# Kernel optimization log

Hardware: AMD Instinct MI355X
Metric: run time of the kernel (lower is better)

The kernel has to match this reference:

```python
import jax, jax.numpy as jnp
import numpy as np

T, H, NH, NKV, HD = 2048, 2048, 16, 4, 128
I, E, TOPK = 4096, 8, 2
EPS = 1e-5
THETA = 10000.0
NEG = -1e9


def rmsnorm(x, w):
    return x * jax.lax.rsqrt(jnp.mean(x * x, axis=-1, keepdims=True) + EPS) * w


def apply_rope(x, pos):
    # neox-style rotary: split head_dim in halves
    half = HD // 2
    inv_freq = 1.0 / (THETA ** (jnp.arange(half, dtype=jnp.float32) / half))
    f = pos.astype(jnp.float32)[:, None] * inv_freq[None, :]      # [T, half]
    cos = jnp.cos(f)[:, None, :]
    sin = jnp.sin(f)[:, None, :]
    x1, x2 = jnp.split(x, 2, axis=-1)
    return jnp.concatenate([x1 * cos - x2 * sin, x2 * cos + x1 * sin], axis=-1)


def setup_inputs() -> dict:
    key = jax.random.key(0)
    ks = jax.random.split(key, 10)
    s = 0.02
    return {
        "positions": jnp.arange(T, dtype=jnp.int32),
        "hidden_states": jax.random.normal(ks[0], (T, H), jnp.float32),
        "residual": jax.random.normal(ks[1], (T, H), jnp.float32),
        "ln1_w": jnp.ones((H,), jnp.float32),
        "ln2_w": jnp.ones((H,), jnp.float32),
        "wq": jax.random.normal(ks[2], (NH * HD, H), jnp.float32) * s,
        "wk": jax.random.normal(ks[3], (NKV * HD, H), jnp.float32) * s,
        "wv": jax.random.normal(ks[4], (NKV * HD, H), jnp.float32) * s,
        "wo": jax.random.normal(ks[5], (H, NH * HD), jnp.float32) * s,
        "gate_w": jax.random.normal(ks[6], (E, H), jnp.float32) * s,
        "w1": jax.random.normal(ks[7], (E, I, H), jnp.float32) * s,
        "w3": jax.random.normal(ks[8], (E, I, H), jnp.float32) * s,
        "w2": jax.random.normal(ks[9], (E, H, I), jnp.float32) * s,
    }


def reference(positions, hidden_states, residual, ln1_w, ln2_w,
              wq, wk, wv, wo, gate_w, w1, w3, w2):
    # fused add + input RMSNorm (vLLM RMSNorm with residual)
    x = hidden_states + residual
    residual = x
    h = rmsnorm(x, ln1_w)

    # attention: QKV proj, RoPE, GQA causal attention, o_proj
    q = (h @ wq.T).reshape(T, NH, HD)
    k = (h @ wk.T).reshape(T, NKV, HD)
    v = (h @ wv.T).reshape(T, NKV, HD)
    q = apply_rope(q, positions)
    k = apply_rope(k, positions)
    rep = NH // NKV
    k = jnp.repeat(k, rep, axis=1)  # [T, NH, HD]
    v = jnp.repeat(v, rep, axis=1)
    scores = jnp.einsum('qhd,khd->hqk', q, k) * (HD ** -0.5)
    causal = jnp.tril(jnp.ones((T, T), bool))
    scores = jnp.where(causal[None, :, :], scores, NEG)
    attn = jax.nn.softmax(scores, axis=-1)
    o = jnp.einsum('hqk,khd->qhd', attn, v).reshape(T, NH * HD)
    o = o @ wo.T

    # fused add + post-attention RMSNorm
    x = o + residual
    residual = x
    h = rmsnorm(x, ln2_w)

    # MoE: router top-k (renormalized) + SwiGLU experts
    logits = h @ gate_w.T                       # [T, E]
    probs = jax.nn.softmax(logits, axis=-1)
    top_w, top_i = jax.lax.top_k(probs, TOPK)
    top_w = top_w / jnp.sum(top_w, axis=-1, keepdims=True)
    coef = jnp.zeros((T, E), h.dtype).at[jnp.arange(T)[:, None], top_i].set(top_w)
    out = jnp.zeros_like(h)
    for e in range(E):
        g = h @ w1[e].T                          # [T, I]
        u = h @ w3[e].T
        out = out + coef[:, e:e + 1] * ((jax.nn.silu(g) * u) @ w2[e].T)
    return (out, residual)
```

## Files before the change

### kernel.cpp

```cpp
#include <hip/hip_runtime.h>
#include <hip/hip_bf16.h>
#include <math.h>


#define T_  2048
#define H_  2048
#define NH  16
#define NKV 4
#define HD  128
#define II_ 4096
#define NE  8
#define EPS 1e-5f
#define PROWS 6144

typedef __bf16 bf16x8 __attribute__((ext_vector_type(8)));
typedef float  f32x4  __attribute__((ext_vector_type(4)));
typedef unsigned short u16;

__device__ __forceinline__ u16 f2b(float f){ __bf16 b = (__bf16)f; return __builtin_bit_cast(u16, b); }
__device__ __forceinline__ float b2f(u16 u){ return (float)__builtin_bit_cast(__bf16, u); }

__device__ __forceinline__ void gll16(const void* g, void* l){
  __builtin_amdgcn_global_load_lds(
      (const __attribute__((address_space(1))) unsigned int*)g,
      (__attribute__((address_space(3))) unsigned int*)l, 16, 0, 0);
}

__device__ __forceinline__ bf16x8 cvt8(f32x4 a, f32x4 b){
  uint4 u;
  u.x = (unsigned)f2b(a[0]) | ((unsigned)f2b(a[1])<<16);
  u.y = (unsigned)f2b(a[2]) | ((unsigned)f2b(a[3])<<16);
  u.z = (unsigned)f2b(b[0]) | ((unsigned)f2b(b[1])<<16);
  u.w = (unsigned)f2b(b[2]) | ((unsigned)f2b(b[3])<<16);
  return __builtin_bit_cast(bf16x8, u);
}

__global__ __launch_bounds__(256) void mx_cvt(const float* __restrict__ s,
                                              u16* __restrict__ d, int n8)
{
  int i = blockIdx.x*256 + threadIdx.x;
  int stride = gridDim.x*256;
  for (; i < n8; i += stride){
    const f32x4* p = (const f32x4*)s + 2*(size_t)i;
    f32x4 a = p[0], b = p[1];
    uint4 u;
    u.x = (unsigned)f2b(a[0]) | ((unsigned)f2b(a[1])<<16);
    u.y = (unsigned)f2b(a[2]) | ((unsigned)f2b(a[3])<<16);
    u.z = (unsigned)f2b(b[0]) | ((unsigned)f2b(b[1])<<16);
    u.w = (unsigned)f2b(b[2]) | ((unsigned)f2b(b[3])<<16);
    ((uint4*)d)[i] = u;
  }
}

__global__ __launch_bounds__(256) void mx_cvt_split(const float* __restrict__ s,
                                                    u16* __restrict__ hi,
                                                    u16* __restrict__ lo, int n8)
{
  int i = blockIdx.x*256 + threadIdx.x;
  int stride = gridDim.x*256;
  for (; i < n8; i += stride){
    const f32x4* p = (const f32x4*)s + 2*(size_t)i;
    f32x4 a = p[0], b = p[1];
    uint4 uh, ul;
    u16 h0,h1,h2,h3;
    h0=f2b(a[0]); h1=f2b(a[1]); h2=f2b(a[2]); h3=f2b(a[3]);
    uh.x = (unsigned)h0 | ((unsigned)h1<<16);
    uh.y = (unsigned)h2 | ((unsigned)h3<<16);
    ul.x = (unsigned)f2b(a[0]-b2f(h0)) | ((unsigned)f2b(a[1]-b2f(h1))<<16);
    ul.y = (unsigned)f2b(a[2]-b2f(h2)) | ((unsigned)f2b(a[3]-b2f(h3))<<16);
    h0=f2b(b[0]); h1=f2b(b[1]); h2=f2b(b[2]); h3=f2b(b[3]);
    uh.z = (unsigned)h0 | ((unsigned)h1<<16);
    uh.w = (unsigned)h2 | ((unsigned)h3<<16);
    ul.z = (unsigned)f2b(b[0]-b2f(h0)) | ((unsigned)f2b(b[1]-b2f(h1))<<16);
    ul.w = (unsigned)f2b(b[2]-b2f(h2)) | ((unsigned)f2b(b[3]-b2f(h3))<<16);
    ((uint4*)hi)[i] = uh;
    ((uint4*)lo)[i] = ul;
  }
}

__global__ void mx_rope_table(const int* __restrict__ pos, float* __restrict__ cosT,
                              float* __restrict__ sinT)
{
  int i = blockIdx.x*256 + threadIdx.x;
  int t = i >> 6, d = i & 63;
  float inv = (float)exp(-((double)d/64.0) * 9.210340371976184);
  float f = (float)pos[t] * inv;
  cosT[i] = cosf(f); sinT[i] = sinf(f);
}

__global__ __launch_bounds__(256) void mx_addnorm(
    const float* __restrict__ a, const float* __restrict__ b,
    const float* __restrict__ gam, float* __restrict__ res_out,
    u16* __restrict__ hi, u16* __restrict__ lo,
    float* __restrict__ hf, u16* __restrict__ hbf, int* __restrict__ mz)
{
  int t = blockIdx.x, tid = threadIdx.x;
  if (mz && t == 0 && tid < 8) mz[tid] = 0;
  const float4* A4 = (const float4*)a + (size_t)t*512;
  const float4* B4 = (const float4*)b + (size_t)t*512;
  float4 va = A4[tid], vb = B4[tid];
  float4 x0; x0.x=va.x+vb.x; x0.y=va.y+vb.y; x0.z=va.z+vb.z; x0.w=va.w+vb.w;
  va = A4[tid+256]; vb = B4[tid+256];
  float4 x1; x1.x=va.x+vb.x; x1.y=va.y+vb.y; x1.z=va.z+vb.z; x1.w=va.w+vb.w;
  float ss = x0.x*x0.x + x0.y*x0.y + x0.z*x0.z + x0.w*x0.w
           + x1.x*x1.x + x1.y*x1.y + x1.z*x1.z + x1.w*x1.w;
  #pragma unroll
  for (int d=32; d; d>>=1) ss += __shfl_down(ss, d);
  __shared__ float red[4];
  if ((tid&63)==0) red[tid>>6] = ss;
  __syncthreads();
  ss = red[0]+red[1]+red[2]+red[3];
  float scale = rsqrtf(ss * (1.f/2048.f) + EPS);
  float4* R4 = (float4*)res_out + (size_t)t*512;
  R4[tid] = x0; R4[tid+256] = x1;
  const float4* G4p = (const float4*)gam;
  float4 g0 = G4p[tid], g1 = G4p[tid+256];
  float4 y0; y0.x=x0.x*scale*g0.x; y0.y=x0.y*scale*g0.y; y0.z=x0.z*scale*g0.z; y0.w=x0.w*scale*g0.w;
  float4 y1; y1.x=x1.x*scale*g1.x; y1.y=x1.y*scale*g1.y; y1.z=x1.z*scale*g1.z; y1.w=x1.w*scale*g1.w;
  if (hf){ float4* H4 = (float4*)hf + (size_t)t*512; H4[tid]=y0; H4[tid+256]=y1; }
  if (hi){
    ushort4 uh, ul;
    uh.x=f2b(y0.x); ul.x=f2b(y0.x-b2f(uh.x));
    uh.y=f2b(y0.y); ul.y=f2b(y0.y-b2f(uh.y));
    uh.z=f2b(y0.z); ul.z=f2b(y0.z-b2f(uh.z));
    uh.w=f2b(y0.w); ul.w=f2b(y0.w-b2f(uh.w));
    ((ushort4*)hi)[(size_t)t*512 + tid] = uh; ((ushort4*)lo)[(size_t)t*512 + tid] = ul;
    uh.x=f2b(y1.x); ul.x=f2b(y1.x-b2f(uh.x));
    uh.y=f2b(y1.y); ul.y=f2b(y1.y-b2f(uh.y));
    uh.z=f2b(y1.z); ul.z=f2b(y1.z-b2f(uh.z));
    uh.w=f2b(y1.w); ul.w=f2b(y1.w-b2f(uh.w));
    ((ushort4*)hi)[(size_t)t*512 + tid+256] = uh; ((ushort4*)lo)[(size_t)t*512 + tid+256] = ul;
  }
  if (hbf){
    ushort4 u0; u0.x=f2b(y0.x); u0.y=f2b(y0.y); u0.z=f2b(y0.z); u0.w=f2b(y0.w);
    ushort4 u1; u1.x=f2b(y1.x); u1.y=f2b(y1.y); u1.z=f2b(y1.z); u1.w=f2b(y1.w);
    ((ushort4*)hbf)[(size_t)t*512 + tid] = u0; ((ushort4*)hbf)[(size_t)t*512 + tid+256] = u1;
  }
}

template<int NX, int NY>
__global__ __launch_bounds__(256,2) void mx_gemm3g(
    const u16* __restrict__ Ah, const u16* __restrict__ Al,
    const u16* __restrict__ Bh, const u16* __restrict__ Bl,
    float* __restrict__ C, int ldc, int K)
{
  __shared__ u16 AhS[128*64], AlS[128*64], BhS[128*64], BlS[128*64];
  int bid = blockIdx.x;
  int xcd = bid & 7, j = bid >> 3;
  int x = j % NX, p = j / NX;
  int y = xcd + 8*p;
  int m0 = x*128, n0 = y*128;
  int tid = threadIdx.x;
  int w = tid>>6, lane = tid&63, wr = w>>1, wc = w&1, g = lane>>4, lr = lane&15;
  f32x4 acc[4][4];
  #pragma unroll
  for (int fm=0;fm<4;fm++)
    #pragma unroll
    for (int fn=0;fn<4;fn++) acc[fm][fn] = (f32x4){0.f,0.f,0.f,0.f};

  for (int k0 = 0; k0 < K; k0 += 64) {
    #pragma unroll
    for (int i=0;i<4;i++){
      int c = i*256 + tid, r = c>>3, ch = c&7;
      int sw = ((ch ^ (r&7))<<3);
      int db = (i*256 + w*64)<<3;
      gll16(Ah + (size_t)(m0+r)*K + k0 + sw, &AhS[db]);
      gll16(Al + (size_t)(m0+r)*K + k0 + sw, &AlS[db]);
      gll16(Bh + (size_t)(n0+r)*K + k0 + sw, &BhS[db]);
      gll16(Bl + (size_t)(n0+r)*K + k0 + sw, &BlS[db]);
    }
    __syncthreads();
    #pragma unroll
    for (int kk=0;kk<2;kk++){
      bf16x8 ah[4], al[4], bh[4], bl[4];
      #pragma unroll
      for (int fm=0;fm<4;fm++){
        int r = wr*64 + fm*16 + lr;
        int ch = ((kk<<2)+g) ^ (r&7);
        ah[fm] = *(const bf16x8*)(&AhS[(r<<6)+(ch<<3)]);
        al[fm] = *(const bf16x8*)(&AlS[(r<<6)+(ch<<3)]);
      }
      #pragma unroll
      for (int fn=0;fn<4;fn++){
        int r = wc*64 + fn*16 + lr;
        int ch = ((kk<<2)+g) ^ (r&7);
        bh[fn] = *(const bf16x8*)(&BhS[(r<<6)+(ch<<3)]);
        bl[fn] = *(const bf16x8*)(&BlS[(r<<6)+(ch<<3)]);
      }
      __builtin_amdgcn_s_setprio(1);
      #pragma unroll
      for (int fm=0;fm<4;fm++)
        #pragma unroll
        for (int fn=0;fn<4;fn++){
          acc[fm][fn] = __builtin_amdgcn_mfma_f32_16x16x32_bf16(ah[fm], bh[fn], acc[fm][fn],0,0,0);
          acc[fm][fn] = __builtin_amdgcn_mfma_f32_16x16x32_bf16(ah[fm], bl[fn], acc[fm][fn],0,0,0);
          acc[fm][fn] = __builtin_amdgcn_mfma_f32_16x16x32_bf16(al[fm], bh[fn], acc[fm][fn],0,0,0);
        }
      __builtin_amdgcn_s_setprio(0);
    }
    __syncthreads();
  }
  #pragma unroll
  for (int fm=0;fm<4;fm++)
    #pragma unroll
    for (int fn=0;fn<4;fn++)
      #pragma unroll
      for (int i=0;i<4;i++){
        size_t rg = (size_t)(m0 + wr*64 + fm*16 + g*4 + i);
        int cg = n0 + wc*64 + fn*16 + lr;
        C[rg*ldc + cg] = acc[fm][fn][i];
      }
}

template<int NX, int NY>
__global__ __launch_bounds__(256) void mx_gemm3(
    const u16* __restrict__ Ah, const u16* __restrict__ Al, int lda,
    const float* __restrict__ B,
    float* __restrict__ C, int ldc, int K)
{
  const int LDT = 72;
  __shared__ u16 Ash[128*LDT], Asl[128*LDT], Bsh[128*LDT], Bsl[128*LDT];
  int bid = blockIdx.x, x, y;
  if constexpr ((NY & 7) == 0) {
    int xcd = bid & 7, j = bid >> 3;
    x = j % NX; int p = j / NX;
    y = xcd + 8*p;
  } else { x = bid % NX; y = bid / NX; }
  int m0 = x*128, n0 = y*128;
  int tid = threadIdx.x;
  int w = tid>>6, lane = tid&63, wr = w>>1, wc = w&1, g = lane>>4, lr = lane&15;
  f32x4 acc[4][4];
  #pragma unroll
  for (int fm=0;fm<4;fm++)
    #pragma unroll
    for (int fn=0;fn<4;fn++) acc[fm][fn] = (f32x4){0.f,0.f,0.f,0.f};
  for (int k0 = 0; k0 < K; k0 += 64) {
    #pragma unroll
    for (int i=0;i<4;i++){
      int c = i*256 + tid, r = c>>3, ch = c&7;
      *(uint4*)(&Ash[r*LDT + ch*8]) = *(const uint4*)(Ah + (size_t)(m0+r)*lda + k0 + ch*8);
      *(uint4*)(&Asl[r*LDT + ch*8]) = *(const uint4*)(Al + (size_t)(m0+r)*lda + k0 + ch*8);
    }
    #pragma unroll
    for (int i=0;i<8;i++){
      int f = i*256 + tid, r = f>>4, c4 = f&15;
      float4 v = *(const float4*)(B + (size_t)(n0+r)*K + k0 + c4*4);
      ushort4 hv, lv;
      hv.x=f2b(v.x); lv.x=f2b(v.x-b2f(hv.x));
      hv.y=f2b(v.y); lv.y=f2b(v.y-b2f(hv.y));
      hv.z=f2b(v.z); lv.z=f2b(v.z-b2f(hv.z));
      hv.w=f2b(v.w); lv.w=f2b(v.w-b2f(hv.w));
      *(ushort4*)(&Bsh[r*LDT + c4*4]) = hv;
      *(ushort4*)(&Bsl[r*LDT + c4*4]) = lv;
    }
    __syncthreads();
    #pragma unroll
    for (int kk=0;kk<2;kk++){
      bf16x8 ah[4], al[4], bh[4], bl[4];
      #pragma unroll
      for (int fm=0;fm<4;fm++){
        int r = wr*64 + fm*16 + lr;
        ah[fm] = *(const bf16x8*)(&Ash[r*LDT + kk*32 + g*8]);
        al[fm] = *(const bf16x8*)(&Asl[r*LDT + kk*32 + g*8]);
      }
      #pragma unroll
      for (int fn=0;fn<4;fn++){
        int r = wc*64 + fn*16 + lr;
        bh[fn] = *(const bf16x8*)(&Bsh[r*LDT + kk*32 + g*8]);
        bl[fn] = *(const bf16x8*)(&Bsl[r*LDT + kk*32 + g*8]);
      }
      __builtin_amdgcn_s_setprio(1);
      #pragma unroll
      for (int fm=0;fm<4;fm++)
        #pragma unroll
        for (int fn=0;fn<4;fn++){
          acc[fm][fn] = __builtin_amdgcn_mfma_f32_16x16x32_bf16(ah[fm], bh[fn], acc[fm][fn],0,0,0);
          acc[fm][fn] = __builtin_amdgcn_mfma_f32_16x16x32_bf16(ah[fm], bl[fn], acc[fm][fn],0,0,0);
          acc[fm][fn] = __builtin_amdgcn_mfma_f32_16x16x32_bf16(al[fm], bh[fn], acc[fm][fn],0,0,0);
        }
      __builtin_amdgcn_s_setprio(0);
    }
    __syncthreads();
  }
  #pragma unroll
  for (int fm=0;fm<4;fm++)
    #pragma unroll
    for (int fn=0;fn<4;fn++)
      #pragma unroll
      for (int i=0;i<4;i++){
        size_t rg = (size_t)(m0 + wr*64 + fm*16 + g*4 + i);
        int cg = n0 + wc*64 + fn*16 + lr;
        C[rg*ldc + cg] = acc[fm][fn][i];
      }
}

template<int NY>
__global__ __launch_bounds__(256,2) void mx_moe_w13(
    const u16* __restrict__ A,
    const u16* __restrict__ B1, const u16* __restrict__ B3,
    u16* __restrict__ Y,
    const int* __restrict__ row_map, const int* __restrict__ meta)
{
  __shared__ u16 As[2][128*32], B1s[2][128*32], B3s[2][128*32];
  int bid = blockIdx.x;
  int xcd = bid & 7, j = bid >> 3;
  int x = j & 15, p = j >> 4;
  int panel = xcd + 8*p;
  int e = panel / NY, y = panel % NY;
  if (x >= meta[16+e]) return;
  int rowbase = meta[8+e] + (x<<7);
  const u16* B1p = B1 + ((size_t)e*II_ + y*128)*H_;
  const u16* B3p = B3 + ((size_t)e*II_ + y*128)*H_;
  int tid = threadIdx.x;
  int w = tid>>6, lane = tid&63, wr = w>>1, wc = w&1, g = lane>>4, lr = lane&15;

  int c0 = tid,       r0 = c0>>2, h0 = ((c0&3) ^ ((r0>>1)&3))<<3;
  int c1 = 256 + tid, r1 = c1>>2, h1 = ((c1&3) ^ ((r1>>1)&3))<<3;
  int grow0 = row_map[rowbase + r0];
  int grow1 = row_map[rowbase + r1];
  const u16* sA0  = A   + (size_t)grow0*H_ + h0;
  const u16* sA1  = A   + (size_t)grow1*H_ + h1;
  const u16* sB10 = B1p + (size_t)r0*H_ + h0;
  const u16* sB11 = B1p + (size_t)r1*H_ + h1;
  const u16* sB30 = B3p + (size_t)r0*H_ + h0;
  const u16* sB31 = B3p + (size_t)r1*H_ + h1;
  int db0 = (w*64)<<3, db1 = (256 + w*64)<<3;

  f32x4 acc1[4][4], acc3[4][4];
  #pragma unroll
  for (int fm=0;fm<4;fm++)
    #pragma unroll
    for (int fn=0;fn<4;fn++){ acc1[fm][fn]=(f32x4){0,0,0,0}; acc3[fm][fn]=(f32x4){0,0,0,0}; }

  auto stage = [&](int buf, int k0){
    gll16(sA0  + k0, &As[buf][db0]);
    gll16(sA1  + k0, &As[buf][db1]);
    gll16(sB10 + k0, &B1s[buf][db0]);
    gll16(sB11 + k0, &B1s[buf][db1]);
    gll16(sB30 + k0, &B3s[buf][db0]);
    gll16(sB31 + k0, &B3s[buf][db1]);
  };
  auto compute = [&](int buf){
    bf16x8 af[4], b1f[4], b3f[4];
    #pragma unroll
    for (int fm=0;fm<4;fm++){
      int r = wr*64 + fm*16 + lr;
      int ch = g ^ ((r>>1)&3);
      af[fm] = *(const bf16x8*)(&As[buf][r*32 + (ch<<3)]);
    }
    #pragma unroll
    for (int fn=0;fn<4;fn++){
      int r = wc*64 + fn*16 + lr;
      int ch = g ^ ((r>>1)&3);
      b1f[fn] = *(const bf16x8*)(&B1s[buf][r*32 + (ch<<3)]);
      b3f[fn] = *(const bf16x8*)(&B3s[buf][r*32 + (ch<<3)]);
    }
    __builtin_amdgcn_s_setprio(1);
    #pragma unroll
    for (int fm=0;fm<4;fm++)
      #pragma unroll
      for (int fn=0;fn<4;fn++){
        acc1[fm][fn] = __builtin_amdgcn_mfma_f32_16x16x32_bf16(af[fm], b1f[fn], acc1[fm][fn],0,0,0);
        acc3[fm][fn] = __builtin_amdgcn_mfma_f32_16x16x32_bf16(af[fm], b3f[fn], acc3[fm][fn],0,0,0);
      }
    __builtin_amdgcn_s_setprio(0);
  };

  const int nt = H_ >> 5;
  stage(0, 0);
  for (int t=0; t<nt; ++t){
    int cur = t & 1;
    if (t+1 < nt){
      stage(cur^1, (t+1)<<5);
      asm volatile("s_waitcnt vmcnt(6)" ::: "memory");
    } else {
      asm volatile("s_waitcnt vmcnt(0)" ::: "memory");
    }
    __builtin_amdgcn_s_barrier();
    compute(cur);
    asm volatile("s_waitcnt lgkmcnt(0)" ::: "memory");
    __builtin_amdgcn_s_barrier();
  }

  int n0 = y*128 + wc*64;
  #pragma unroll
  for (int fm=0;fm<4;fm++)
    #pragma unroll
    for (int fn=0;fn<4;fn++)
      #pragma unroll
      for (int i=0;i<4;i++){
        size_t rg = (size_t)(rowbase + wr*64 + fm*16 + g*4 + i);
        int cg = n0 + fn*16 + lr;
        float gg = acc1[fm][fn][i], uu = acc3[fm][fn][i];
        float sg = gg / (1.f + __expf(-gg));
        Y[rg*II_ + cg] = f2b(sg * uu);
      }
}

template<int NY>
__global__ __launch_bounds__(256,2) void mx_moe_w2k(
    const u16* __restrict__ A,
    const u16* __restrict__ B,
    float* __restrict__ C,
    const int* __restrict__ meta)
{
  __shared__ u16 As[128*64], Bs[128*64];
  int bid = blockIdx.x;
  int xcd = bid & 7, j = bid >> 3;
  int x = j & 15, p = j >> 4;
  int panel = xcd + 8*p;
  int e = panel / NY, y = panel % NY;
  if (x >= meta[16+e]) return;
  int rowbase = meta[8+e] + (x<<7);
  const u16* Bp = B + ((size_t)e*H_ + y*128)*II_;
  int tid = threadIdx.x;
  int w = tid>>6, lane = tid&63, wr = w>>1, wc = w&1, g = lane>>4, lr = lane&15;

  f32x4 acc[4][4];
  #pragma unroll
  for (int fm=0;fm<4;fm++)
    #pragma unroll
    for (int fn=0;fn<4;fn++) acc[fm][fn] = (f32x4){0,0,0,0};

  for (int k0 = 0; k0 < II_; k0 += 64) {
    #pragma unroll
    for (int i=0;i<4;i++){
      int c = i*256 + tid, r = c>>3, ch = c&7;
      int sw = (ch ^ (r&7))<<3;
      int db = (i*256 + w*64)<<3;
      gll16(A  + (size_t)(rowbase + r)*II_ + k0 + sw, &As[db]);
      gll16(Bp + (size_t)r*II_             + k0 + sw, &Bs[db]);
    }
    __syncthreads();
    #pragma unroll
    for (int kk=0;kk<2;kk++){
      bf16x8 af[4], bf[4];
      #pragma unroll
      for (int fm=0;fm<4;fm++){
        int r = wr*64 + fm*16 + lr;
        int ch = ((kk<<2)+g) ^ (r&7);
        af[fm] = *(const bf16x8*)(&As[(r<<6)+(ch<<3)]);
      }
      #pragma unroll
      for (int fn=0;fn<4;fn++){
        int r = wc*64 + fn*16 + lr;
        int ch = ((kk<<2)+g) ^ (r&7);
        bf[fn] = *(const bf16x8*)(&Bs[(r<<6)+(ch<<3)]);
      }
      __builtin_amdgcn_s_setprio(1);
      #pragma unroll
      for (int fm=0;fm<4;fm++)
        #pragma unroll
        for (int fn=0;fn<4;fn++)
          acc[fm][fn] = __builtin_amdgcn_mfma_f32_16x16x32_bf16(af[fm], bf[fn], acc[fm][fn],0,0,0);
      __builtin_amdgcn_s_setprio(0);
    }
    __syncthreads();
  }
  int n0 = y*128 + wc*64;
  #pragma unroll
  for (int fm=0;fm<4;fm++)
    #pragma unroll
    for (int fn=0;fn<4;fn++)
      #pragma unroll
      for (int i=0;i<4;i++){
        size_t rg = (size_t)(rowbase + wr*64 + fm*16 + g*4 + i);
        int cg = n0 + fn*16 + lr;
        C[rg*H_ + cg] = acc[fm][fn][i];
      }
}

template<int GATHER, int CBF16, int NYT, int SPLITY>
__global__ __launch_bounds__(512,4) void mx_moe10(
    const u16* __restrict__ A, int lda,
    const float* __restrict__ B1, const float* __restrict__ B2, long long strideB,
    void* __restrict__ C1v, void* __restrict__ C2v, int ldc, int K,
    const int* __restrict__ row_map, const int* __restrict__ meta)
{
  __shared__ u16 AS[3][256*32];
  int bid = blockIdx.x;
  int xcd = bid & 7, j = bid >> 3;
  int x = j & 7, q = j >> 3;
  int panel = xcd + 8*q;
  int e = panel / NYT, y = panel % NYT;
  if (x >= meta[16+e]) return;
  int rowbase = meta[8+e] + x*256;
  int yy = (y < SPLITY) ? y : y - SPLITY;
  const float* Bp = ((y < SPLITY) ? B1 : B2) + (long long)e*strideB + (size_t)(yy*128)*K;
  void* Cv = (y < SPLITY) ? C1v : C2v;
  int tid = threadIdx.x;
  int w = tid>>6, lane = tid&63, wr = w>>2, wc = w&3, g = lane>>4, lr = lane&15;
  const u16 *srcA0, *srcA1;
  {
    int c0 = tid,     r0 = c0>>2;
    int c1 = 512+tid, r1 = c1>>2;
    int s0 = (c0&3) ^ ((r0>>1)&3);
    int s1 = (c1&3) ^ ((r1>>1)&3);
    int w0 = GATHER ? row_map[rowbase+r0] : (rowbase+r0);
    int w1r = GATHER ? row_map[rowbase+r1] : (rowbase+r1);
    srcA0 = A + (size_t)w0*lda + s0*8;
    srcA1 = A + (size_t)w1r*lda + s1*8;
  }
  const float *srcB0, *srcB1;
  {
    int r0 = wc*32 + lr;
    int r1 = wc*32 + 16 + lr;
    srcB0 = Bp + (size_t)r0*K + g*8;
    srcB1 = Bp + (size_t)r1*K + g*8;
  }
  f32x4 acc[8][2];
  #pragma unroll
  for (int fm=0;fm<8;fm++){ acc[fm][0]=(f32x4){0,0,0,0}; acc[fm][1]=(f32x4){0,0,0,0}; }
  f32x4 e0,e1,e2,e3, o0,o1,o2,o3;
  u16 *pa0=&AS[0][0], *pa1=&AS[1][0], *pa2=&AS[2][0];
  int nt = K >> 5;
  auto stageA = [&](u16* as, int k0){
    gll16(srcA0 + k0, as + (w*64)*8);
    gll16(srcA1 + k0, as + (512 + w*64)*8);
  };
  auto issueB = [&](int k0, f32x4& b0, f32x4& b1, f32x4& b2, f32x4& b3){
    b0 = *(const f32x4*)(srcB0 + k0);
    b1 = *(const f32x4*)(srcB0 + k0 + 4);
    b2 = *(const f32x4*)(srcB1 + k0);
    b3 = *(const f32x4*)(srcB1 + k0 + 4);
  };
  auto compute = [&](const u16* as, f32x4 b0, f32x4 b1, f32x4 b2, f32x4 b3){
    bf16x8 bf0 = cvt8(b0,b1), bf1 = cvt8(b2,b3);
    __builtin_amdgcn_s_setprio(1);
    #pragma unroll
    for (int fm=0;fm<8;fm++){
      int r = wr*128 + fm*16 + lr;
      int ch = g ^ ((r>>1)&3);
      bf16x8 af = *(const bf16x8*)(as + r*32 + ch*8);
      acc[fm][0] = __builtin_amdgcn_mfma_f32_16x16x32_bf16(af, bf0, acc[fm][0],0,0,0);
      acc[fm][1] = __builtin_amdgcn_mfma_f32_16x16x32_bf16(af, bf1, acc[fm][1],0,0,0);
    }
    __builtin_amdgcn_s_setprio(0);
  };
  auto rot = [&](){ u16* t0=pa0; pa0=pa1; pa1=pa2; pa2=t0; };
  auto kclamp = [&](int t){ return (t < nt ? t : 0) << 5; };
  issueB(0, e0,e1,e2,e3);
  asm volatile("" ::: "memory");
  stageA(pa0, 0);
  asm volatile("" ::: "memory");
  stageA(pa1, kclamp(1));
  for (int t=0; t<nt; t+=2){
    asm volatile("s_waitcnt vmcnt(2)" ::: "memory");
    __builtin_amdgcn_s_barrier();
    issueB(kclamp(t+1), o0,o1,o2,o3);
    asm volatile("" ::: "memory");
    stageA(pa2, kclamp(t+2));
    compute(pa0, e0,e1,e2,e3);
    rot();
    asm volatile("s_waitcnt vmcnt(2)" ::: "memory");
    __builtin_amdgcn_s_barrier();
    issueB(kclamp(t+2), e0,e1,e2,e3);
    asm volatile("" ::: "memory");
    stageA(pa2, kclamp(t+3));
    compute(pa0, o0,o1,o2,o3);
    rot();
  }
  int n0 = yy*128 + wc*32;
  #pragma unroll
  for (int fm=0;fm<8;fm++)
    #pragma unroll
    for (int fn=0;fn<2;fn++)
      #pragma unroll
      for (int i=0;i<4;i++){
        size_t rg = (size_t)(rowbase + wr*128 + fm*16 + g*4 + i);
        int cg = n0 + fn*16 + lr;
        if (CBF16) ((u16*)Cv)[rg*ldc + cg] = f2b(acc[fm][fn][i]);
        else       ((float*)Cv)[rg*ldc + cg] = acc[fm][fn][i];
      }
}

__global__ __launch_bounds__(256) void mx_rope_apply(const float* __restrict__ qkv,
    const float* __restrict__ cosT, const float* __restrict__ sinT,
    u16* __restrict__ qh, u16* __restrict__ ql, u16* __restrict__ kh, u16* __restrict__ kl)
{
  int t = blockIdx.x*4 + (threadIdx.x>>6);
  int hh = blockIdx.y, d = threadIdx.x & 63;
  const float* row = qkv + (size_t)t*3072;
  float c = cosT[t*64+d], s = sinT[t*64+d];
  float x1, x2; size_t base; u16 *oh, *ol;
  if (hh < NH){ x1 = row[hh*HD+d]; x2 = row[hh*HD+d+64];
     base = ((size_t)hh*T_ + t)*HD; oh = qh; ol = ql; }
  else { int kvh = hh-NH; x1 = row[2048 + kvh*HD + d]; x2 = row[2048 + kvh*HD + d + 64];
     base = ((size_t)kvh*T_ + t)*HD; oh = kh; ol = kl; }
  float o1 = x1*c - x2*s, o2 = x2*c + x1*s;
  u16 a = f2b(o1); oh[base+d]    = a; ol[base+d]    = f2b(o1 - b2f(a));
  u16 b = f2b(o2); oh[base+d+64] = b; ol[base+d+64] = f2b(o2 - b2f(b));
}

__global__ void mx_transpose_v(const float* __restrict__ qkv,
                               u16* __restrict__ vh, u16* __restrict__ vl)
{
  __shared__ float tile[64][132];
  int kv = blockIdx.x, t0 = blockIdx.y*64, tid = threadIdx.x;
  #pragma unroll
  for (int it=0; it<32; ++it){
    int idx = it*256 + tid; int r = idx>>7, d = idx&127;
    tile[r][d] = qkv[(size_t)(t0+r)*3072 + 2560 + kv*HD + d];
  }
  __syncthreads();
  #pragma unroll
  for (int it=0; it<32; ++it){
    int idx = it*256 + tid; int d = idx>>6, j = idx&63;
    float x = tile[j][d];
    u16 a = f2b(x);
    size_t o = ((size_t)kv*HD + d)*T_ + t0 + j;
    vh[o] = a; vl[o] = f2b(x - b2f(a));
  }
}

__global__ __launch_bounds__(256) void mx_attn(
  const u16* __restrict__ qh_, const u16* __restrict__ ql_,
  const u16* __restrict__ kh_, const u16* __restrict__ kl_,
  const u16* __restrict__ vh_, const u16* __restrict__ vl_,
  u16* __restrict__ oh_, u16* __restrict__ ol_)
{
  int h = blockIdx.y, kvh = h >> 2;
  int qt = (h & 8) ? (31 - (int)blockIdx.x) : (int)blockIdx.x;
  int tid = threadIdx.x, w = tid>>6, lane = tid&63, g = lane>>4, lr = lane&15;
  int q0 = qt*64 + w*16;
  __shared__ u16 KV[2][4][8192];
  __shared__ u16 Ph[4][1024], Pl[4][1024];

  bf16x8 qfh[4], qfl[4];
  const u16* qrh = qh_ + ((size_t)h*T_ + q0 + lr)*HD;
  const u16* qrl = ql_ + ((size_t)h*T_ + q0 + lr)*HD;
  #pragma unroll
  for (int kk=0;kk<4;kk++){
    qfh[kk] = *(const bf16x8*)(qrh + kk*32 + g*8);
    qfl[kk] = *(const bf16x8*)(qrl + kk*32 + g*8);
  }
  f32x4 o[8];
  #pragma unroll
  for (int nf=0;nf<8;nf++) o[nf] = (f32x4){0.f,0.f,0.f,0.f};
  float mreg[4] = {-3e38f,-3e38f,-3e38f,-3e38f}, lsum[4] = {0.f,0.f,0.f,0.f};

  const u16* kbase = kh_ + (size_t)kvh*T_*HD;
  const u16* lbase = kl_ + (size_t)kvh*T_*HD;
  const u16* vbase = vh_ + (size_t)kvh*HD*T_;
  const u16* wbase = vl_ + (size_t)kvh*HD*T_;

  auto stage = [&](int buf, int kvb){
    #pragma unroll
    for (int i=0;i<4;i++){
      int cb = i*256 + w*64;
      int c  = cb + lane;
      int kr = c>>4, kc = ((c&15) ^ (kr&7))<<3;
      gll16(kbase + (size_t)(kvb+kr)*HD + kc, &KV[buf][0][cb*8]);
      gll16(lbase + (size_t)(kvb+kr)*HD + kc, &KV[buf][1][cb*8]);
      int vr = c>>3, vc = ((c&7) ^ (vr&7))<<3;
      gll16(vbase + (size_t)vr*T_ + kvb + vc, &KV[buf][2][cb*8]);
      gll16(wbase + (size_t)vr*T_ + kvb + vc, &KV[buf][3][cb*8]);
    }
  };

  stage(0, 0);

  for (int kt = 0; kt <= qt; ++kt) {
    int cur = kt & 1;
    int kvb = kt*64;
    if (kt < qt) {
      stage(cur^1, kvb+64);
      asm volatile("s_waitcnt vmcnt(16)" ::: "memory");
    } else {
      asm volatile("s_waitcnt vmcnt(0)" ::: "memory");
    }
    __builtin_amdgcn_s_barrier();

    f32x4 s[4];
    #pragma unroll
    for (int nf=0;nf<4;nf++) s[nf] = (f32x4){0.f,0.f,0.f,0.f};
    __builtin_amdgcn_s_setprio(1);
    #pragma unroll
    for (int nf=0; nf<4; nf++){
      int row = nf*16 + lr;
      #pragma unroll
      for (int kk=0;kk<4;kk++){
        int off = row*128 + ((((kk<<2)+g) ^ (lr&7))<<3);
        bf16x8 kf = *(const bf16x8*)(&KV[cur][0][off]);
        bf16x8 kg = *(const bf16x8*)(&KV[cur][1][off]);
        s[nf] = __builtin_amdgcn_mfma_f32_16x16x32_bf16(qfh[kk], kf, s[nf],0,0,0);
        s[nf] = __builtin_amdgcn_mfma_f32_16x16x32_bf16(qfh[kk], kg, s[nf],0,0,0);
        s[nf] = __builtin_amdgcn_mfma_f32_16x16x32_bf16(qfl[kk], kf, s[nf],0,0,0);
      }
    }
    __builtin_amdgcn_s_setprio(0);

    float sv[4][4], pm[4];
    #pragma unroll
    for (int i=0;i<4;i++) pm[i] = -3e38f;
    bool diag = (kt == qt);
    #pragma unroll
    for (int nf=0;nf<4;nf++)
      #pragma unroll
      for (int i=0;i<4;i++){
        float v = s[nf][i] * 0.08838834764831845f;
        if (diag && (kvb + nf*16 + lr > q0 + g*4 + i)) v = -1e30f;
        sv[nf][i] = v;
        pm[i] = fmaxf(pm[i], v);
      }
    #pragma unroll
    for (int i=0;i<4;i++)
      #pragma unroll
      for (int d=1; d<16; d<<=1) pm[i] = fmaxf(pm[i], __shfl_xor(pm[i], d));
    float sf[4], psum[4];
    #pragma unroll
    for (int i=0;i<4;i++){
      float nm = fmaxf(mreg[i], pm[i]);
      sf[i] = __expf(mreg[i] - nm);
      mreg[i] = nm; psum[i] = 0.f;
    }
    #pragma unroll
    for (int nf=0;nf<4;nf++)
      #pragma unroll
      for (int i=0;i<4;i++){
        float e = __expf(sv[nf][i] - mreg[i]);
        sv[nf][i] = e; psum[i] += e;
      }
    #pragma unroll
    for (int i=0;i<4;i++){
      #pragma unroll
      for (int d=1; d<16; d<<=1) psum[i] += __shfl_xor(psum[i], d);
      lsum[i] = lsum[i]*sf[i] + psum[i];
    }
    #pragma unroll
    for (int nf=0;nf<8;nf++)
      #pragma unroll
      for (int i=0;i<4;i++) o[nf][i] *= sf[i];

    #pragma unroll
    for (int nf=0;nf<4;nf++)
      #pragma unroll
      for (int i=0;i<4;i++){
        int qi = g*4 + i, kv = nf*16 + lr;
        int idx = qi*64 + (kv ^ ((qi&7)<<3));
        u16 hb = f2b(sv[nf][i]);
        Ph[w][idx] = hb;
        Pl[w][idx] = f2b(sv[nf][i] - b2f(hb));
      }

    #pragma unroll
    for (int kk2=0; kk2<2; kk2++){
      int pidx = lr*64 + ((kk2*32 + g*8) ^ ((lr&7)<<3));
      bf16x8 ph = *(const bf16x8*)(&Ph[w][pidx]);
      bf16x8 pl = *(const bf16x8*)(&Pl[w][pidx]);
      __builtin_amdgcn_s_setprio(1);
      #pragma unroll
      for (int nf=0; nf<8; nf++){
        int row = nf*16 + lr;
        int off = row*64 + ((((kk2<<2)+g) ^ (lr&7))<<3);
        bf16x8 vf = *(const bf16x8*)(&KV[cur][2][off]);
        bf16x8 vg = *(const bf16x8*)(&KV[cur][3][off]);
        o[nf] = __builtin_amdgcn_mfma_f32_16x16x32_bf16(ph, vf, o[nf],0,0,0);
        o[nf] = __builtin_amdgcn_mfma_f32_16x16x32_bf16(ph, vg, o[nf],0,0,0);
        o[nf] = __builtin_amdgcn_mfma_f32_16x16x32_bf16(pl, vf, o[nf],0,0,0);
      }
      __builtin_amdgcn_s_setprio(0);
    }
    __builtin_amdgcn_s_barrier();
  }

  float inv[4];
  #pragma unroll
  for (int i=0;i<4;i++) inv[i] = 1.0f / lsum[i];
  #pragma unroll
  for (int nf=0;nf<8;nf++)
    #pragma unroll
    for (int i=0;i<4;i++){
      float v = o[nf][i] * inv[i];
      size_t oidx = (size_t)(q0 + g*4 + i)*2048 + h*HD + nf*16 + lr;
      u16 hb = f2b(v);
      oh_[oidx] = hb; ol_[oidx] = f2b(v - b2f(hb));
    }
}

__global__ __launch_bounds__(256) void mx_router(
    const float* __restrict__ h2, const float* __restrict__ gw,
    int* __restrict__ meta, int* __restrict__ tki, float* __restrict__ tkw)
{
  int t = blockIdx.x, tid = threadIdx.x;
  float p[8] = {0,0,0,0,0,0,0,0};
  const float* row = h2 + (size_t)t*H_;
  for (int i = tid; i < H_; i += 256) {
    float x = row[i];
    #pragma unroll
    for (int e=0;e<8;e++) p[e] += x * gw[e*H_ + i];
  }
  #pragma unroll
  for (int e=0;e<8;e++)
    #pragma unroll
    for (int d=32; d; d>>=1) p[e] += __shfl_down(p[e], d);
  __shared__ float red[4][8];
  int w = tid>>6;
  if ((tid&63)==0){
    #pragma unroll
    for (int e=0;e<8;e++) red[w][e] = p[e];
  }
  __syncthreads();
  if (tid==0){
    float lg[8];
    #pragma unroll
    for (int e=0;e<8;e++) lg[e] = red[0][e]+red[1][e]+red[2][e]+red[3][e];
    int e0 = 0;
    for (int e=1;e<8;e++) if (lg[e] > lg[e0]) e0 = e;
    int e1 = (e0==0)?1:0;
    for (int e=0;e<8;e++) if (e!=e0 && lg[e] > lg[e1]) e1 = e;
    float w0 = 1.f/(1.f + __expf(lg[e1]-lg[e0]));
    tki[t*2]=e0; tki[t*2+1]=e1; tkw[t*2]=w0; tkw[t*2+1]=1.f-w0;
    atomicAdd(&meta[e0],1); atomicAdd(&meta[e1],1);
  }
}

__global__ void mx_scan(int* __restrict__ meta, int* __restrict__ perm, int gsh)
{
  if (threadIdx.x == 0){
    int run = 0;
    for (int e=0;e<8;e++){
      meta[8+e] = run;
      int pt = (meta[e] + (1<<gsh) - 1) >> gsh;
      meta[16+e] = pt;
      run += pt << gsh;
      meta[24+e] = 0;
    }
  }
  for (int i = threadIdx.x; i < PROWS; i += 256) perm[i] = 0;
}

__global__ void mx_scatter(const int* __restrict__ tki, int* __restrict__ meta,
                           int* __restrict__ perm, int* __restrict__ slot)
{
  int t = blockIdx.x*256 + threadIdx.x;
  if (t >= T_) return;
  #pragma unroll
  for (int j=0;j<2;j++){
    int e = tki[t*2+j];
    int s = atomicAdd(&meta[24+e], 1);
    int pos = meta[8+e] + s;
    perm[pos] = t;
    slot[t*2+j] = pos;
  }
}

__global__ void mx_silu(u16* __restrict__ y1, const u16* __restrict__ y3)
{
  size_t base = ((size_t)blockIdx.x*256 + threadIdx.x)*8;
  uint4 a = *(uint4*)(y1+base);
  uint4 b = *(const uint4*)(y3+base);
  u16* ap = (u16*)&a; u16* bp = (u16*)&b;
  uint4 r; u16* rp = (u16*)&r;
  #pragma unroll
  for (int j=0;j<8;j++){
    float gg = b2f(ap[j]), uu = b2f(bp[j]);
    float sg = gg / (1.f + __expf(-gg));
    rp[j] = f2b(sg * uu);
  }
  *(uint4*)(y1+base) = r;
}

__global__ void mx_combine(const float* __restrict__ Y2, const int* __restrict__ slot,
                           const float* __restrict__ tkw, float* __restrict__ out)
{
  int t = blockIdx.x, tid = threadIdx.x;
  int s0 = slot[t*2], s1 = slot[t*2+1];
  float w0 = tkw[t*2], w1 = tkw[t*2+1];
  const float4* r0 = (const float4*)(Y2 + (size_t)s0*H_);
  const float4* r1 = (const float4*)(Y2 + (size_t)s1*H_);
  float4* o4 = (float4*)(out + (size_t)t*H_);
  for (int i = tid; i < 512; i += 256){
    float4 a = r0[i], b = r1[i], c;
    c.x = w0*a.x + w1*b.x; c.y = w0*a.y + w1*b.y;
    c.z = w0*a.z + w1*b.z; c.w = w0*a.w + w1*b.w;
    o4[i] = c;
  }
}

extern "C" void kernel_launch(void* const* d_in, const int* in_sizes, int n_in,
                              void* d_out, int out_size, void* d_ws, size_t ws_size,
                              hipStream_t stream)
{
  (void)in_sizes; (void)n_in; (void)out_size;
  const int*   positions = (const int*)  d_in[0];
  const float* hidden    = (const float*)d_in[1];
  const float* residual  = (const float*)d_in[2];
  const float* ln1       = (const float*)d_in[3];
  const float* ln2       = (const float*)d_in[4];
  const float* wq        = (const float*)d_in[5];
  const float* wk        = (const float*)d_in[6];
  const float* wv        = (const float*)d_in[7];
  const float* wo        = (const float*)d_in[8];
  const float* gatew     = (const float*)d_in[9];
  const float* w1        = (const float*)d_in[10];
  const float* w3        = (const float*)d_in[11];
  const float* w2        = (const float*)d_in[12];
  float* outp = (float*)d_out;
  char* ws = (char*)d_ws;

  size_t off = 0;
  auto alloc = [&](size_t n){ size_t o = off; off += (n + 255) & ~(size_t)255; return o; };
  float* cosT = (float*)(ws + alloc((size_t)T_*64*4));
  float* sinT = (float*)(ws + alloc((size_t)T_*64*4));
  size_t res1_off = alloc((size_t)T_*H_*4);
  float* res1 = (float*)(ws + res1_off);
  u16*   h1h  = (u16*)  (ws + alloc((size_t)T_*H_*2));
  u16*   h1l  = (u16*)  (ws + alloc((size_t)T_*H_*2));
  float* qkvF = (float*)(ws + alloc((size_t)T_*3072*4));
  size_t qh_off = alloc((size_t)NH*T_*HD*2);
  u16*   qh   = (u16*)  (ws + qh_off);
  u16*   ql   = (u16*)  (ws + alloc((size_t)NH*T_*HD*2));
  u16*   kh   = (u16*)  (ws + alloc((size_t)NKV*T_*HD*2));
  u16*   kl   = (u16*)  (ws + alloc((size_t)NKV*T_*HD*2));
  u16*   vh   = (u16*)  (ws + alloc((size_t)NKV*T_*HD*2));
  u16*   vl   = (u16*)  (ws + alloc((size_t)NKV*T_*HD*2));
  u16*   aoh  = (u16*)  (ws + alloc((size_t)T_*2048*2));
  u16*   aol  = (u16*)  (ws + alloc((size_t)T_*2048*2));
  float* oF   = (float*)(ws + alloc((size_t)T_*H_*4));
  float* h2f  = (float*)(ws + alloc((size_t)T_*H_*4));
  u16*   h2b  = (u16*)  (ws + alloc((size_t)T_*H_*2));
  int*   meta = (int*)  (ws + alloc(32*4));
  int*   tki  = (int*)  (ws + alloc((size_t)T_*2*4));
  float* tkw  = (float*)(ws + alloc((size_t)T_*2*4));
  int*   slot = (int*)  (ws + alloc((size_t)T_*2*4));
  int*   perm = (int*)  (ws + alloc((size_t)PROWS*4));
  u16*   Y1   = (u16*)  (ws + alloc((size_t)PROWS*II_*2));
  u16*   Y3   = (u16*)  (ws + res1_off);
  float* Y2   = (float*)(ws + qh_off);
  u16* w1b = (u16*)(ws + alloc((size_t)NE*II_*H_*2));
  u16* w3b = (u16*)(ws + alloc((size_t)NE*II_*H_*2));
  u16* w2b = (u16*)(ws + alloc((size_t)NE*H_*II_*2));
  u16* qwh = (u16*)(ws + alloc((size_t)3072*H_*2));
  u16* qwl = (u16*)(ws + alloc((size_t)3072*H_*2));
  u16* woh = (u16*)(ws + alloc((size_t)H_*H_*2));
  u16* wol = (u16*)(ws + alloc((size_t)H_*H_*2));
  bool big = ws_size >= off;

  if (big){
    int n8 = NE*II_*H_/8;
    mx_cvt<<<2048, 256, 0, stream>>>(w1, w1b, n8);
    mx_cvt<<<2048, 256, 0, stream>>>(w3, w3b, n8);
    mx_cvt<<<2048, 256, 0, stream>>>(w2, w2b, n8);
    mx_cvt_split<<<512, 256, 0, stream>>>(wq, qwh,                qwl,                2048*2048/8);
    mx_cvt_split<<<512, 256, 0, stream>>>(wk, qwh + 2048*2048,    qwl + 2048*2048,    512*2048/8);
    mx_cvt_split<<<512, 256, 0, stream>>>(wv, qwh + 2560*2048,    qwl + 2560*2048,    512*2048/8);
    mx_cvt_split<<<512, 256, 0, stream>>>(wo, woh,                wol,                2048*2048/8);
  }
  mx_rope_table<<<512, 256, 0, stream>>>(positions, cosT, sinT);
  mx_addnorm<<<T_, 256, 0, stream>>>(hidden, residual, ln1, res1, h1h, h1l,
                                     nullptr, nullptr, nullptr);
  if (big){
    mx_gemm3g<16,24><<<384, 256, 0, stream>>>(h1h, h1l, qwh, qwl, qkvF, 3072, H_);
  } else {
    mx_gemm3<16,16><<<256, 256, 0, stream>>>(h1h, h1l, H_, wq, qkvF,        3072, H_);
    mx_gemm3<16, 4><<< 64, 256, 0, stream>>>(h1h, h1l, H_, wk, qkvF + 2048, 3072, H_);
    mx_gemm3<16, 4><<< 64, 256, 0, stream>>>(h1h, h1l, H_, wv, qkvF + 2560, 3072, H_);
  }
  mx_rope_apply<<<dim3(T_/4, NH+NKV), 256, 0, stream>>>(qkvF, cosT, sinT, qh, ql, kh, kl);
  mx_transpose_v<<<dim3(NKV, T_/64), 256, 0, stream>>>(qkvF, vh, vl);
  mx_attn<<<dim3(T_/64, NH), 256, 0, stream>>>(qh, ql, kh, kl, vh, vl, aoh, aol);
  if (big){
    mx_gemm3g<16,16><<<256, 256, 0, stream>>>(aoh, aol, woh, wol, oF, 2048, 2048);
  } else {
    mx_gemm3<16,16><<<256, 256, 0, stream>>>(aoh, aol, 2048, wo, oF, H_, 2048);
  }
  mx_addnorm<<<T_, 256, 0, stream>>>(oF, res1, ln2, outp + (size_t)T_*H_,
                                     nullptr, nullptr, h2f, h2b, meta);
  mx_router<<<T_, 256, 0, stream>>>(h2f, gatew, meta, tki, tkw);
  mx_scan<<<1, 256, 0, stream>>>(meta, perm, big ? 7 : 8);
  mx_scatter<<<T_/256, 256, 0, stream>>>(tki, meta, perm, slot);
  if (big){
    mx_moe_w13<32><<<4096, 256, 0, stream>>>(h2b, w1b, w3b, Y1, perm, meta);
    mx_moe_w2k<16><<<2048, 256, 0, stream>>>(Y1, w2b, Y2, meta);
  } else {
    mx_moe10<1,1,64,32><<<4096, 512, 0, stream>>>(h2b, H_, w1, w3, (long long)II_*H_,
                                                  Y1, Y3, II_, H_, perm, meta);
    mx_silu<<<(PROWS*II_/8)/256, 256, 0, stream>>>(Y1, Y3);
    mx_moe10<0,0,16,16><<<1024, 512, 0, stream>>>(Y1, II_, w2, w2, (long long)H_*II_,
                                                  Y2, Y2, H_, II_, perm, meta);
  }
  mx_combine<<<T_, 256, 0, stream>>>(Y2, slot, tkw, outp);
}
```

Before: 1.114 ms.

## Single-buffer MoE w13 with BK=64 and load attention low-parts directly from global

```diff
diff --git a/kernel.cpp b/kernel.cpp
--- a/kernel.cpp
+++ b/kernel.cpp
@@ -301,7 +301,7 @@
     u16* __restrict__ Y,
     const int* __restrict__ row_map, const int* __restrict__ meta)
 {
-  __shared__ u16 As[2][128*32], B1s[2][128*32], B3s[2][128*32];
+  __shared__ u16 As[128*64], B1s[128*64], B3s[128*64];
   int bid = blockIdx.x;
   int xcd = bid & 7, j = bid >> 3;
   int x = j & 15, p = j >> 4;
@@ -314,74 +314,52 @@
   int tid = threadIdx.x;
   int w = tid>>6, lane = tid&63, wr = w>>1, wc = w&1, g = lane>>4, lr = lane&15;
 
-  int c0 = tid,       r0 = c0>>2, h0 = ((c0&3) ^ ((r0>>1)&3))<<3;
-  int c1 = 256 + tid, r1 = c1>>2, h1 = ((c1&3) ^ ((r1>>1)&3))<<3;
-  int grow0 = row_map[rowbase + r0];
-  int grow1 = row_map[rowbase + r1];
-  const u16* sA0  = A   + (size_t)grow0*H_ + h0;
-  const u16* sA1  = A   + (size_t)grow1*H_ + h1;
-  const u16* sB10 = B1p + (size_t)r0*H_ + h0;
-  const u16* sB11 = B1p + (size_t)r1*H_ + h1;
-  const u16* sB30 = B3p + (size_t)r0*H_ + h0;
-  const u16* sB31 = B3p + (size_t)r1*H_ + h1;
-  int db0 = (w*64)<<3, db1 = (256 + w*64)<<3;
-
   f32x4 acc1[4][4], acc3[4][4];
   #pragma unroll
   for (int fm=0;fm<4;fm++)
     #pragma unroll
     for (int fn=0;fn<4;fn++){ acc1[fm][fn]=(f32x4){0,0,0,0}; acc3[fm][fn]=(f32x4){0,0,0,0}; }
 
-  auto stage = [&](int buf, int k0){
-    gll16(sA0  + k0, &As[buf][db0]);
-    gll16(sA1  + k0, &As[buf][db1]);
-    gll16(sB10 + k0, &B1s[buf][db0]);
-    gll16(sB11 + k0, &B1s[buf][db1]);
-    gll16(sB30 + k0, &B3s[buf][db0]);
-    gll16(sB31 + k0, &B3s[buf][db1]);
-  };
-  auto compute = [&](int buf){
-    bf16x8 af[4], b1f[4], b3f[4];
-    #pragma unroll
-    for (int fm=0;fm<4;fm++){
-      int r = wr*64 + fm*16 + lr;
-      int ch = g ^ ((r>>1)&3);
-      af[fm] = *(const bf16x8*)(&As[buf][r*32 + (ch<<3)]);
-    }
-    #pragma unroll
-    for (int fn=0;fn<4;fn++){
-      int r = wc*64 + fn*16 + lr;
-      int ch = g ^ ((r>>1)&3);
-      b1f[fn] = *(const bf16x8*)(&B1s[buf][r*32 + (ch<<3)]);
-      b3f[fn] = *(const bf16x8*)(&B3s[buf][r*32 + (ch<<3)]);
-    }
-    __builtin_amdgcn_s_setprio(1);
-    #pragma unroll
-    for (int fm=0;fm<4;fm++)
+  for (int k0 = 0; k0 < H_; k0 += 64) {
+    #pragma unroll
+    for (int i=0;i<4;i++){
+      int c = i*256 + tid, r = c>>3, ch = c&7;
+      int sw = (ch ^ (r&7))<<3;
+      int db = (i*256 + w*64)<<3;
+      int grow = row_map[rowbase + r];
+      gll16(A   + (size_t)grow*H_ + k0 + sw, &As[db]);
+      gll16(B1p + (size_t)r*H_    + k0 + sw, &B1s[db]);
+      gll16(B3p + (size_t)r*H_    + k0 + sw, &B3s[db]);
+    }
+    __syncthreads();
+    #pragma unroll
+    for (int kk=0;kk<2;kk++){
+      bf16x8 af[4], b1f[4], b3f[4];
+      #pragma unroll
+      for (int fm=0;fm<4;fm++){
+        int r = wr*64 + fm*16 + lr;
+        int ch = ((kk<<2)+g) ^ (r&7);
+        af[fm] = *(const bf16x8*)(&As[(r<<6)+(ch<<3)]);
+      }
       #pragma unroll
       for (int fn=0;fn<4;fn++){
-        acc1[fm][fn] = __builtin_amdgcn_mfma_f32_16x16x32_bf16(af[fm], b1f[fn], acc1[fm][fn],0,0,0);
-        acc3[fm][fn] = __builtin_amdgcn_mfma_f32_16x16x32_bf16(af[fm], b3f[fn], acc3[fm][fn],0,0,0);
-      }
-    __builtin_amdgcn_s_setprio(0);
-  };
-
-  const int nt = H_ >> 5;
-  stage(0, 0);
-  for (int t=0; t<nt; ++t){
-    int cur = t & 1;
-    if (t+1 < nt){
-      stage(cur^1, (t+1)<<5);
-      asm volatile("s_waitcnt vmcnt(6)" ::: "memory");
-    } else {
-      asm volatile("s_waitcnt vmcnt(0)" ::: "memory");
-    }
-    __builtin_amdgcn_s_barrier();
-    compute(cur);
-    asm volatile("s_waitcnt lgkmcnt(0)" ::: "memory");
-    __builtin_amdgcn_s_barrier();
-  }
-
+        int r = wc*64 + fn*16 + lr;
+        int ch = ((kk<<2)+g) ^ (r&7);
+        b1f[fn] = *(const bf16x8*)(&B1s[(r<<6)+(ch<<3)]);
+        b3f[fn] = *(const bf16x8*)(&B3s[(r<<6)+(ch<<3)]);
+      }
+      __builtin_amdgcn_s_setprio(1);
+      #pragma unroll
+      for (int fm=0;fm<4;fm++)
+        #pragma unroll
+        for (int fn=0;fn<4;fn++){
+          acc1[fm][fn] = __builtin_amdgcn_mfma_f32_16x16x32_bf16(af[fm], b1f[fn], acc1[fm][fn],0,0,0);
+          acc3[fm][fn] = __builtin_amdgcn_mfma_f32_16x16x32_bf16(af[fm], b3f[fn], acc3[fm][fn],0,0,0);
+        }
+      __builtin_amdgcn_s_setprio(0);
+    }
+    __syncthreads();
+  }
   int n0 = y*128 + wc*64;
   #pragma unroll
   for (int fm=0;fm<4;fm++)
@@ -623,7 +601,7 @@
   int qt = (h & 8) ? (31 - (int)blockIdx.x) : (int)blockIdx.x;
   int tid = threadIdx.x, w = tid>>6, lane = tid&63, g = lane>>4, lr = lane&15;
   int q0 = qt*64 + w*16;
-  __shared__ u16 KV[2][4][8192];
+  __shared__ u16 KV[2][2][8192];
   __shared__ u16 Ph[4][1024], Pl[4][1024];
 
   bf16x8 qfh[4], qfl[4];
@@ -651,10 +629,8 @@
       int c  = cb + lane;
       int kr = c>>4, kc = ((c&15) ^ (kr&7))<<3;
       gll16(kbase + (size_t)(kvb+kr)*HD + kc, &KV[buf][0][cb*8]);
-      gll16(lbase + (size_t)(kvb+kr)*HD + kc, &KV[buf][1][cb*8]);
       int vr = c>>3, vc = ((c&7) ^ (vr&7))<<3;
-      gll16(vbase + (size_t)vr*T_ + kvb + vc, &KV[buf][2][cb*8]);
-      gll16(wbase + (size_t)vr*T_ + kvb + vc, &KV[buf][3][cb*8]);
+      gll16(vbase + (size_t)vr*T_ + kvb + vc, &KV[buf][1][cb*8]);
     }
   };
 
@@ -665,7 +641,7 @@
     int kvb = kt*64;
     if (kt < qt) {
       stage(cur^1, kvb+64);
-      asm volatile("s_waitcnt vmcnt(16)" ::: "memory");
+      asm volatile("s_waitcnt vmcnt(8)" ::: "memory");
     } else {
       asm volatile("s_waitcnt vmcnt(0)" ::: "memory");
     }
@@ -678,11 +654,12 @@
     #pragma unroll
     for (int nf=0; nf<4; nf++){
       int row = nf*16 + lr;
+      const u16* krl = lbase + (size_t)(kvb + row)*HD;
       #pragma unroll
       for (int kk=0;kk<4;kk++){
         int off = row*128 + ((((kk<<2)+g) ^ (lr&7))<<3);
         bf16x8 kf = *(const bf16x8*)(&KV[cur][0][off]);
-        bf16x8 kg = *(const bf16x8*)(&KV[cur][1][off]);
+        bf16x8 kg = *(const bf16x8*)(krl + kk*32 + g*8);
         s[nf] = __builtin_amdgcn_mfma_f32_16x16x32_bf16(qfh[kk], kf, s[nf],0,0,0);
         s[nf] = __builtin_amdgcn_mfma_f32_16x16x32_bf16(qfh[kk], kg, s[nf],0,0,0);
         s[nf] = __builtin_amdgcn_mfma_f32_16x16x32_bf16(qfl[kk], kf, s[nf],0,0,0);
@@ -753,8 +730,8 @@
       for (int nf=0; nf<8; nf++){
         int row = nf*16 + lr;
         int off = row*64 + ((((kk2<<2)+g) ^ (lr&7))<<3);
-        bf16x8 vf = *(const bf16x8*)(&KV[cur][2][off]);
-        bf16x8 vg = *(const bf16x8*)(&KV[cur][3][off]);
+        bf16x8 vf = *(const bf16x8*)(&KV[cur][1][off]);
+        bf16x8 vg = *(const bf16x8*)(wbase + (size_t)row*T_ + kvb + kk2*32 + g*8);
         o[nf] = __builtin_amdgcn_mfma_f32_16x16x32_bf16(ph, vf, o[nf],0,0,0);
         o[nf] = __builtin_amdgcn_mfma_f32_16x16x32_bf16(ph, vg, o[nf],0,0,0);
         o[nf] = __builtin_amdgcn_mfma_f32_16x16x32_bf16(pl, vf, o[nf],0,0,0);
```

Measured after the change: 1.286 ms. +15.5%, slower.
